# Optimization experiments

Measured on AMD Instinct MI355X. Metric: run time of the kernel, lower is better.

Reference implementation:

```python
import jax, jax.numpy as jnp
import numpy as np
from jax import lax

BS, T, H, V, E, NREG, SEQ = 1024, 10, 256, 50000, 50, 1, 50
EPS = 1e-5


def _edge_index(bs):
    # get_batch_graph(max_len=10, windows=3): per graph, edges[0:-1] of combinations keeps
    # (j-3, j-2) and (j-3, j-1) for j in 3..10, plus (8,9) and (9,0). 18 edges/graph.
    e = []
    for j in range(3, 11):
        e += [(j - 3, j - 2), (j - 3, j - 1)]
    e += [(8, 9), (9, 0)]
    e = np.asarray(e, dtype=np.int32)                      # [18, 2]
    e = (e[None] + 10 * np.arange(bs, dtype=np.int32)[:, None, None]).reshape(-1, 2)
    return jnp.asarray(e[:, 0]), jnp.asarray(e[:, 1])      # src, dst


def setup_inputs() -> dict:
    key = jax.random.key(0)
    ks = jax.random.split(key, 24)
    s = 0.02
    inp = {
        'lags': jax.random.normal(ks[0], (BS, T), jnp.float32),
        'weather': jax.random.normal(ks[1], (BS, T, 2), jnp.float32),
        'event': jax.random.normal(ks[2], (BS, T, 4), jnp.float32),
        'text': jax.random.randint(ks[3], (BS, T, SEQ), 0, V, jnp.int32),
        'emb': jax.random.normal(ks[4], (V, E), jnp.float32) * s,
        'conv3_w': jax.random.normal(ks[5], (H // 2, E, 3), jnp.float32) * s,
        'conv3_b': jnp.zeros((H // 2,), jnp.float32),
        'conv4_w': jax.random.normal(ks[6], (H // 2, H // 2, 4), jnp.float32) * s,
        'conv4_b': jnp.zeros((H // 2,), jnp.float32),
        'lags_w': jax.random.normal(ks[7], (H, 1), jnp.float32) * s,
        'lags_b': jnp.zeros((H,), jnp.float32),
        'weather_w': jax.random.normal(ks[8], (H, 2), jnp.float32) * s,
        'weather_b': jnp.zeros((H,), jnp.float32),
        'event_w': jax.random.normal(ks[9], (H, 4), jnp.float32) * s,
        'event_b': jnp.zeros((H,), jnp.float32),
        'text_w': jax.random.normal(ks[10], (H, H // 2), jnp.float32) * s,
        'text_b': jnp.zeros((H,), jnp.float32),
        'merge_w': jax.random.normal(ks[11], (H, 4 * H), jnp.float32) * s,
        'merge_b': jnp.zeros((H,), jnp.float32),
        'bn_gamma': jnp.ones((H,), jnp.float32),
        'bn_beta': jnp.zeros((H,), jnp.float32),
        'mh_w': jax.random.normal(ks[12], (H, H), jnp.float32) * s,
        'mh_b': jnp.zeros((H,), jnp.float32),
        'gru_wih': jax.random.normal(ks[13], (3 * H, H), jnp.float32) * s,
        'gru_whh': jax.random.normal(ks[14], (3 * H, H), jnp.float32) * s,
        'gru_bih': jnp.zeros((3 * H,), jnp.float32),
        'gru_bhh': jnp.zeros((3 * H,), jnp.float32),
        'reg_w': jax.random.normal(ks[15], (NREG, T * H), jnp.float32) * s,
        'reg_b': jnp.zeros((NREG,), jnp.float32),
    }
    return inp


def _conv1d(x, w, b):
    # x: [N, Cin, L], w: [Cout, Cin, K] (torch layout)
    y = lax.conv_general_dilated(x, w, (1,), 'VALID',
                                 dimension_numbers=('NCH', 'OIH', 'NCH'))
    return y + b[None, :, None]


def _forward(lags, weather, event, text, emb, conv3_w, conv3_b, conv4_w, conv4_b,
             lags_w, lags_b, weather_w, weather_b, event_w, event_b, text_w, text_b,
             merge_w, merge_b, bn_gamma, bn_beta, mh_w, mh_b,
             gru_wih, gru_whh, gru_bih, gru_bhh, reg_w, reg_b):
    bs = lags.shape[0]
    n = bs * T
    h = mh_w.shape[0]

    # per-node feature projections
    l = lags.reshape(-1, 1) @ lags_w.T + lags_b                       # [N, H]
    w = weather.reshape(-1, 2) @ weather_w.T + weather_b              # [N, H]
    ev = event.reshape(-1, 4) @ event_w.T + event_b                   # [N, H]

    # text CNN branch (dropout = identity, eval mode)
    tx = emb[text.reshape(-1, SEQ)]                                   # [N, 50, E]
    tx = jnp.transpose(tx, (0, 2, 1))                                 # [N, E, 50]
    c3 = jax.nn.relu(_conv1d(tx, conv3_w, conv3_b))                   # [N, H/2, 48]
    c4 = jax.nn.relu(_conv1d(c3, conv4_w, conv4_b))                   # [N, H/2, 45]
    tx = jnp.max(c4, axis=2)                                          # [N, H/2]
    tx = tx @ text_w.T + text_b                                       # [N, H]

    # message passing: sum mailbox per destination node (all nodes have in-deg >= 1)
    src, dst = _edge_index(bs)
    def agg(f):
        return jax.ops.segment_sum(f[src], dst, num_segments=n)
    hcat = jnp.concatenate([agg(l), agg(w), agg(ev), agg(tx)], axis=-1)  # [N, 4H]

    # fused linear -> relu -> batchnorm (batch stats) -> linear
    m = jax.nn.relu(hcat @ merge_w.T + merge_b)
    mu = jnp.mean(m, axis=0)
    var = jnp.var(m, axis=0)
    m = (m - mu) / jnp.sqrt(var + EPS) * bn_gamma + bn_beta
    m = m @ mh_w.T + mh_b                                             # [N, H]

    # GRU over the 10 lag steps
    hg = m.reshape(bs, T, h)
    def step(hprev, x_t):
        gi = x_t @ gru_wih.T + gru_bih
        gh = hprev @ gru_whh.T + gru_bhh
        r = jax.nn.sigmoid(gi[:, :h] + gh[:, :h])
        z = jax.nn.sigmoid(gi[:, h:2 * h] + gh[:, h:2 * h])
        nn_ = jnp.tanh(gi[:, 2 * h:] + r * gh[:, 2 * h:])
        hnew = (1.0 - z) * nn_ + z * hprev
        return hnew, hnew
    h0 = jnp.zeros((bs, h), m.dtype)
    _, outs = lax.scan(step, h0, jnp.transpose(hg, (1, 0, 2)))        # [T, bs, H]
    out = jnp.transpose(outs, (1, 0, 2)).reshape(bs, -1)              # [bs, T*H]
    return out @ reg_w.T + reg_b                                      # [bs, n_reg]


def reference(lags, weather, event, text, emb, conv3_w, conv3_b, conv4_w, conv4_b,
              lags_w, lags_b, weather_w, weather_b, event_w, event_b, text_w, text_b,
              merge_w, merge_b, bn_gamma, bn_beta, mh_w, mh_b,
              gru_wih, gru_whh, gru_bih, gru_bhh, reg_w, reg_b):
    return _forward(lags, weather, event, text, emb, conv3_w, conv3_b, conv4_w, conv4_b,
                    lags_w, lags_b, weather_w, weather_b, event_w, event_b, text_w, text_b,
                    merge_w, merge_b, bn_gamma, bn_beta, mh_w, mh_b,
                    gru_wih, gru_whh, gru_bih, gru_bhh, reg_w, reg_b)
```

## Files before the change

### kernel.cpp

```cpp
#include <hip/hip_runtime.h>
#include <math.h>


typedef unsigned short u16;
typedef __attribute__((ext_vector_type(8))) short short8v;
typedef __attribute__((ext_vector_type(4))) float float4v;
#define MFMA16 __builtin_amdgcn_mfma_f32_16x16x32_bf16

__device__ inline u16 f2bf(float f) {
  unsigned u = __float_as_uint(f);
  u += 0x7FFFu + ((u >> 16) & 1u);
  return (u16)(u >> 16);
}

__global__ __launch_bounds__(256) void k_zero(float* __restrict__ p, int n) {
  int i = blockIdx.x * 256 + threadIdx.x;
  if (i < n) p[i] = 0.f;
}

__global__ __launch_bounds__(256) void k_repb3(const float* __restrict__ w3,
                                               u16* __restrict__ w3b) {
  int i = blockIdx.x * 256 + threadIdx.x;
  if (i >= 24576) return;
  int j = i & 7, l = (i >> 3) & 63, nt = (i >> 9) & 7, kt = i >> 12;
  int k = kt * 32 + (l >> 4) * 8 + j;
  int c = nt * 16 + (l & 15);
  int kk = k >> 6, e = k & 63;
  float v = (e < 50) ? w3[c * 150 + e * 3 + kk] : 0.f;
  w3b[i] = f2bf(v);
}

__global__ __launch_bounds__(256) void k_repb4(const float* __restrict__ w4,
                                               u16* __restrict__ w4b) {
  int i = blockIdx.x * 256 + threadIdx.x;
  int j = i & 7, l = (i >> 3) & 63, nt = (i >> 9) & 7, kt = i >> 12;
  int k = kt * 32 + (l >> 4) * 8 + j;
  int c = nt * 16 + (l & 15);
  int kk = k >> 7, ci = k & 127;
  w4b[i] = f2bf(w4[c * 512 + ci * 4 + kk]);
}

__global__ __launch_bounds__(256) void k_repwhh(const float* __restrict__ whh,
                                                u16* __restrict__ whhb) {
  int i = blockIdx.x * 256 + threadIdx.x;
  int j = i & 7, l = (i >> 3) & 63, kt = (i >> 9) & 7, nt = i >> 12;
  int n = nt * 16 + (l & 15);
  int k = kt * 32 + (l >> 4) * 8 + j;
  whhb[i] = f2bf(whh[n * 256 + k]);
}

__global__ __launch_bounds__(256) void k_pcomb(const float* __restrict__ wih,
                                               const float* __restrict__ mh_w,
                                               const float* __restrict__ mh_b,
                                               const float* __restrict__ bih,
                                               float* __restrict__ Wcomb,
                                               float* __restrict__ b1) {
  int g0 = blockIdx.x * 8, t = threadIdx.x;
  float acc[8] = {0.f, 0.f, 0.f, 0.f, 0.f, 0.f, 0.f, 0.f};
  for (int j = 0; j < 256; ++j) {
    float wv = mh_w[j * 256 + t];
#pragma unroll
    for (int r = 0; r < 8; ++r) acc[r] += wih[(g0 + r) * 256 + j] * wv;
  }
#pragma unroll
  for (int r = 0; r < 8; ++r) Wcomb[(g0 + r) * 256 + t] = acc[r];
  __shared__ float red[4][8];
  float mb = mh_b[t];
#pragma unroll
  for (int r = 0; r < 8; ++r) {
    float v = wih[(g0 + r) * 256 + t] * mb;
    v += __shfl_down(v, 32); v += __shfl_down(v, 16); v += __shfl_down(v, 8);
    v += __shfl_down(v, 4);  v += __shfl_down(v, 2);  v += __shfl_down(v, 1);
    if ((t & 63) == 0) red[t >> 6][r] = v;
  }
  __syncthreads();
  if (t < 8) b1[g0 + t] = bih[g0 + t] + red[0][t] + red[1][t] + red[2][t] + red[3][t];
}

__global__ __launch_bounds__(256) void k_pmerge(const float* __restrict__ merge_w,
                                                const float* __restrict__ text_w,
                                                const float* __restrict__ lags_w,
                                                const float* __restrict__ weather_w,
                                                const float* __restrict__ event_w,
                                                const float* __restrict__ lags_b,
                                                const float* __restrict__ weather_b,
                                                const float* __restrict__ event_b,
                                                const float* __restrict__ text_b,
                                                float* __restrict__ MtxT,
                                                float* __restrict__ A_l,
                                                float* __restrict__ MwT,
                                                float* __restrict__ MeT,
                                                float* __restrict__ bias_deg) {
  int blk = blockIdx.x, t = threadIdx.x;
  if (blk < 128) {
    int c = blk;
    float acc = 0.f;
    for (int j = 0; j < 256; ++j)
      acc += merge_w[t * 1024 + 768 + j] * text_w[j * 128 + c];
    MtxT[c * 256 + t] = acc;
  } else {
    float a = 0.f, w0 = 0.f, w1 = 0.f, e0 = 0.f, e1 = 0.f, e2 = 0.f, e3 = 0.f, bd = 0.f;
    for (int j = 0; j < 256; ++j) {
      float m0 = merge_w[t * 1024 + j];
      float m1 = merge_w[t * 1024 + 256 + j];
      float m2 = merge_w[t * 1024 + 512 + j];
      float m3 = merge_w[t * 1024 + 768 + j];
      a  += m0 * lags_w[j];
      w0 += m1 * weather_w[j * 2 + 0];
      w1 += m1 * weather_w[j * 2 + 1];
      e0 += m2 * event_w[j * 4 + 0];
      e1 += m2 * event_w[j * 4 + 1];
      e2 += m2 * event_w[j * 4 + 2];
      e3 += m2 * event_w[j * 4 + 3];
      bd += m0 * lags_b[j] + m1 * weather_b[j] + m2 * event_b[j] + m3 * text_b[j];
    }
    A_l[t] = a;
    MwT[t] = w0; MwT[256 + t] = w1;
    MeT[t] = e0; MeT[256 + t] = e1; MeT[512 + t] = e2; MeT[768 + t] = e3;
    bias_deg[t] = bd;
  }
}


#define LOADB(DST, SRC, KT)                                                    \
  _Pragma("unroll") for (int nt = 0; nt < 8; ++nt)                             \
      DST[nt] = *(const short8v*)&SRC[((((KT) * 8 + nt) * 64) + l) * 8];

#define AFRAG3(AF, KT) {                                                       \
    const int kk_ = (KT) >> 1;                                                 \
    const int eb_ = 4 * ((KT) & 1) + g;                                        \
    _Pragma("unroll") for (int mt = 0; mt < 3; ++mt) {                         \
      int pr_ = 16 * mt + lr + kk_;                                            \
      int bb_ = eb_ ^ (pr_ & 7);                                               \
      AF[mt] = *(const short8v*)&sx[pr_ * 64 + bb_ * 8];                       \
    } }

#define AFRAG4(AF, KT) {                                                       \
    const int t4_ = 4 * (KT) + g;                                              \
    const int kk_ = t4_ >> 4;                                                  \
    const int bk_ = t4_ & 15;                                                  \
    _Pragma("unroll") for (int mt = 0; mt < 3; ++mt) {                         \
      int pr_ = 16 * mt + lr + kk_;                                            \
      int bb_ = (bk_ & 8) | ((bk_ ^ pr_) & 7);                                 \
      AF[mt] = *(const short8v*)&sc3[pr_ * 128 + bb_ * 8];                     \
    } }

#define MSTEP(AF, BF)                                                          \
  _Pragma("unroll") for (int nt = 0; nt < 8; ++nt)                             \
    _Pragma("unroll") for (int mt = 0; mt < 3; ++mt)                           \
      acc[mt][nt] = MFMA16(AF[mt], BF[nt], acc[mt][nt], 0, 0, 0);

__global__ __launch_bounds__(64) void k_textcnn(const int* __restrict__ text,
                                                const float* __restrict__ emb,
                                                const u16* __restrict__ w3b,
                                                const float* __restrict__ b3,
                                                const u16* __restrict__ w4b,
                                                const float* __restrict__ b4,
                                                float* __restrict__ mx_g) {
  __shared__ u16 sbuf[52 * 128];
  u16* sx = sbuf;
  u16* sc3 = sbuf;
  const int n = blockIdx.x;
  const int l = threadIdx.x;
  const int lr = l & 15;
  const int g = l >> 4;

  int idxv = (l < 50) ? text[n * 50 + l] : 0;
  const int e = l;
#pragma unroll 10
  for (int s = 0; s < 50; ++s) {
    int id = __shfl(idxv, s);
    float v = (e < 50) ? emb[id * 50 + e] : 0.f;
    int bb = (e >> 3) ^ (s & 7);
    sx[s * 64 + bb * 8 + (e & 7)] = f2bf(v);
  }
  __syncthreads();

  const float4v zv = {0.f, 0.f, 0.f, 0.f};
  float4v acc[3][8];
#pragma unroll
  for (int mt = 0; mt < 3; ++mt)
#pragma unroll
    for (int nt = 0; nt < 8; ++nt) acc[mt][nt] = zv;

  float b3v[8];
#pragma unroll
  for (int nt = 0; nt < 8; ++nt) b3v[nt] = b3[nt * 16 + lr];

  {
    short8v bA[8], bB[8], a[3];
    LOADB(bA, w3b, 0);
    for (int kt = 0; kt < 6; kt += 2) {
      LOADB(bB, w3b, kt + 1);
      AFRAG3(a, kt);
      MSTEP(a, bA);
      if (kt + 2 < 6) LOADB(bA, w3b, kt + 2);
      AFRAG3(a, kt + 1);
      MSTEP(a, bB);
    }
  }
  __syncthreads();

#pragma unroll
  for (int mt = 0; mt < 3; ++mt)
#pragma unroll
    for (int nt = 0; nt < 8; ++nt) {
#pragma unroll
      for (int r = 0; r < 4; ++r) {
        int p = 16 * mt + 4 * g + r;
        int c = 16 * nt + lr;
        float v = fmaxf(acc[mt][nt][r] + b3v[nt], 0.f);
        int bb = (c >> 3) & 15;
        bb = (bb & 8) | ((bb ^ (p & 7)) & 7);
        sc3[p * 128 + bb * 8 + (c & 7)] = f2bf(v);
      }
      acc[mt][nt] = zv;
    }
  __syncthreads();

  {
    short8v bA[8], bB[8], a[3];
    LOADB(bA, w4b, 0);
    for (int kt = 0; kt < 16; kt += 2) {
      LOADB(bB, w4b, kt + 1);
      AFRAG4(a, kt);
      MSTEP(a, bA);
      if (kt + 2 < 16) LOADB(bA, w4b, kt + 2);
      AFRAG4(a, kt + 1);
      MSTEP(a, bB);
    }
  }

#pragma unroll
  for (int nt = 0; nt < 8; ++nt) {
    float m0 = -1e30f;
#pragma unroll
    for (int mt = 0; mt < 3; ++mt)
#pragma unroll
      for (int r = 0; r < 4; ++r) {
        int p = 16 * mt + 4 * g + r;
        if (p < 45) m0 = fmaxf(m0, acc[mt][nt][r]);
      }
    m0 = fmaxf(m0, __shfl_xor(m0, 16));
    m0 = fmaxf(m0, __shfl_xor(m0, 32));
    int c = 16 * nt + lr;
    float bias = b4[c];
    if (g == 0) mx_g[n * 128 + c] = fmaxf(m0 + bias, 0.f);
  }
}

__device__ inline void preds_of(int i, int& p1, int& p2, int& d) {
  int tt = i % 10;
  int base = i - tt;
  if (tt == 0)      { p1 = base + 9;      p2 = -1;             d = 1; }
  else if (tt == 1) { p1 = base;          p2 = -1;             d = 1; }
  else              { p1 = base + tt - 2; p2 = base + tt - 1;  d = 2; }
}

__global__ __launch_bounds__(256) void k_merge(const float* __restrict__ mx_g,
                                               const float* __restrict__ lags,
                                               const float* __restrict__ weather,
                                               const float* __restrict__ event,
                                               const float* __restrict__ MtxT,
                                               const float* __restrict__ A_l,
                                               const float* __restrict__ MwT,
                                               const float* __restrict__ MeT,
                                               const float* __restrict__ bias_deg,
                                               const float* __restrict__ merge_b,
                                               u16* __restrict__ m_bf,
                                               float* __restrict__ bnsum,
                                               float* __restrict__ bnsumsq) {
  __shared__ __align__(16) float mxs[16 * 128];
  __shared__ float scal[16 * 8];
  const int tid = threadIdx.x;
  const int row0 = blockIdx.x * 16;
  for (int idx = tid; idx < 2048; idx += 256) {
    int r = idx >> 7, c = idx & 127;
    int p1, p2, d;
    preds_of(row0 + r, p1, p2, d);
    float v = mx_g[p1 * 128 + c];
    if (p2 >= 0) v += mx_g[p2 * 128 + c];
    mxs[r * 128 + c] = v;
  }
  if (tid < 16) {
    int p1, p2, d;
    preds_of(row0 + tid, p1, p2, d);
    float sl = lags[p1];
    float sw0 = weather[p1 * 2], sw1 = weather[p1 * 2 + 1];
    float se0 = event[p1 * 4], se1 = event[p1 * 4 + 1];
    float se2 = event[p1 * 4 + 2], se3 = event[p1 * 4 + 3];
    if (p2 >= 0) {
      sl += lags[p2];
      sw0 += weather[p2 * 2]; sw1 += weather[p2 * 2 + 1];
      se0 += event[p2 * 4];     se1 += event[p2 * 4 + 1];
      se2 += event[p2 * 4 + 2]; se3 += event[p2 * 4 + 3];
    }
    scal[tid * 8 + 0] = sl;
    scal[tid * 8 + 1] = sw0; scal[tid * 8 + 2] = sw1;
    scal[tid * 8 + 3] = se0; scal[tid * 8 + 4] = se1;
    scal[tid * 8 + 5] = se2; scal[tid * 8 + 6] = se3;
    scal[tid * 8 + 7] = (float)d;
  }
  __syncthreads();
  const int t = tid;
  float acc[16];
#pragma unroll
  for (int r = 0; r < 16; ++r) acc[r] = 0.f;
  for (int c4 = 0; c4 < 32; ++c4) {
    const int c = c4 * 4;
    float w0 = MtxT[c * 256 + t];
    float w1 = MtxT[(c + 1) * 256 + t];
    float w2 = MtxT[(c + 2) * 256 + t];
    float w3 = MtxT[(c + 3) * 256 + t];
#pragma unroll
    for (int r = 0; r < 16; ++r) {
      float4 mv = *(const float4*)&mxs[r * 128 + c];
      acc[r] += mv.x * w0 + mv.y * w1 + mv.z * w2 + mv.w * w3;
    }
  }
  float al = A_l[t], mw0 = MwT[t], mw1 = MwT[256 + t];
  float me0 = MeT[t], me1 = MeT[256 + t], me2 = MeT[512 + t], me3 = MeT[768 + t];
  float bd = bias_deg[t], mb = merge_b[t];
  float s1 = 0.f, s2 = 0.f;
#pragma unroll
  for (int r = 0; r < 16; ++r) {
    float mp = acc[r] + scal[r * 8] * al + scal[r * 8 + 1] * mw0 + scal[r * 8 + 2] * mw1
             + scal[r * 8 + 3] * me0 + scal[r * 8 + 4] * me1 + scal[r * 8 + 5] * me2
             + scal[r * 8 + 6] * me3 + scal[r * 8 + 7] * bd + mb;
    float mv = fmaxf(mp, 0.f);
    m_bf[(row0 + r) * 256 + t] = f2bf(mv);
    s1 += mv;
    s2 += mv * mv;
  }
  atomicAdd(&bnsum[t], s1);
  atomicAdd(&bnsumsq[t], s2);
}

__global__ __launch_bounds__(256) void k_bna(const float* __restrict__ bnsum,
                                             const float* __restrict__ bnsumsq,
                                             const float* __restrict__ gamma,
                                             const float* __restrict__ beta,
                                             float* __restrict__ svec,
                                             float* __restrict__ tvec) {
  int c = threadIdx.x;
  float mu = bnsum[c] * (1.f / 10240.f);
  float var = bnsumsq[c] * (1.f / 10240.f) - mu * mu;
  float s = gamma[c] * rsqrtf(var + 1e-5f);
  svec[c] = s;
  tvec[c] = beta[c] - mu * s;
}

__global__ __launch_bounds__(256) void k_bnbc(const float* __restrict__ Wcomb,
                                              const float* __restrict__ svec,
                                              const float* __restrict__ tvec,
                                              const float* __restrict__ b1,
                                              u16* __restrict__ wbig_b,
                                              float* __restrict__ bias_big) {
  int blk = blockIdx.x, t = threadIdx.x;
  __shared__ float red[4];
  if (blk < 768) {
    int i = blk * 256 + t;
    int j = i & 7, l = (i >> 3) & 63, kt = (i >> 9) & 7, nt = i >> 12;
    int n = nt * 16 + (l & 15);
    int k = kt * 32 + (l >> 4) * 8 + j;
    wbig_b[i] = f2bf(Wcomb[n * 256 + k] * svec[k]);
  } else {
    int gg = blk - 768;
    float part = tvec[t] * Wcomb[gg * 256 + t];
    part += __shfl_down(part, 32); part += __shfl_down(part, 16);
    part += __shfl_down(part, 8);  part += __shfl_down(part, 4);
    part += __shfl_down(part, 2);  part += __shfl_down(part, 1);
    if ((t & 63) == 0) red[t >> 6] = part;
    __syncthreads();
    if (t == 0) bias_big[gg] = b1[gg] + red[0] + red[1] + red[2] + red[3];
  }
}

__global__ __launch_bounds__(256) void k_gi(const u16* __restrict__ m_bf,
                                            const u16* __restrict__ wbig_b,
                                            const float* __restrict__ bias_big,
                                            float* __restrict__ gi) {
  const int t = threadIdx.x;
  const int w = t >> 6, l = t & 63, lr = l & 15, g = l >> 4;
  const int row0 = blockIdx.x * 16;
  short8v a[8];
#pragma unroll
  for (int kt = 0; kt < 8; ++kt)
    a[kt] = *(const short8v*)&m_bf[(row0 + lr) * 256 + kt * 32 + g * 8];
  const float4v zv = {0.f, 0.f, 0.f, 0.f};
  float4v acc[12];
#pragma unroll
  for (int j = 0; j < 12; ++j) acc[j] = zv;
#pragma unroll 2
  for (int kt = 0; kt < 8; ++kt) {
#pragma unroll
    for (int j = 0; j < 12; ++j) {
      int nt = w * 12 + j;
      short8v b = *(const short8v*)&wbig_b[((nt * 8 + kt) * 64 + l) * 8];
      acc[j] = MFMA16(a[kt], b, acc[j], 0, 0, 0);
    }
  }
#pragma unroll
  for (int j = 0; j < 12; ++j) {
    int col = (w * 12 + j) * 16 + lr;
    float bb = bias_big[col];
#pragma unroll
    for (int r = 0; r < 4; ++r)
      gi[(row0 + g * 4 + r) * 768 + col] = acc[j][r] + bb;
  }
}

__global__ __launch_bounds__(256) void k_gru_all(const float* __restrict__ gi,
                                                 const u16* __restrict__ whhb,
                                                 const float* __restrict__ bhh,
                                                 const float* __restrict__ reg_w,
                                                 const float* __restrict__ reg_b,
                                                 float* __restrict__ out) {
  __shared__ u16 hb[16 * 256];
  __shared__ float red[4][16];
  const int t = threadIdx.x;
  const int w = t >> 6, l = t & 63, lr = l & 15, g = l >> 4;
  const int row0 = blockIdx.x * 16;
  for (int i = t; i < 4096; i += 256) hb[i] = 0;
  float hp[4][4];
#pragma unroll
  for (int i = 0; i < 4; ++i)
#pragma unroll
    for (int r = 0; r < 4; ++r) hp[i][r] = 0.f;
  float bh[3][4];
#pragma unroll
  for (int gate = 0; gate < 3; ++gate)
#pragma unroll
    for (int i = 0; i < 4; ++i)
      bh[gate][i] = bhh[gate * 256 + (w * 4 + i) * 16 + lr];
  float racc[4] = {0.f, 0.f, 0.f, 0.f};

  for (int s = 0; s < 10; ++s) {
    __syncthreads();
    const float4v zv = {0.f, 0.f, 0.f, 0.f};
    float4v acc[3][4];
#pragma unroll
    for (int gate = 0; gate < 3; ++gate)
#pragma unroll
      for (int i = 0; i < 4; ++i) acc[gate][i] = zv;
#pragma unroll
    for (int kt = 0; kt < 8; ++kt) {
      int kb = kt * 4 + g;
      int bb = kb ^ (lr & 7);
      short8v a = *(const short8v*)&hb[lr * 256 + bb * 8];
#pragma unroll
      for (int gate = 0; gate < 3; ++gate)
#pragma unroll
        for (int i = 0; i < 4; ++i) {
          int nt = gate * 16 + w * 4 + i;
          short8v b = *(const short8v*)&whhb[((nt * 8 + kt) * 64 + l) * 8];
          acc[gate][i] = MFMA16(a, b, acc[gate][i], 0, 0, 0);
        }
    }
    __syncthreads();
    float rw[4];
#pragma unroll
    for (int i = 0; i < 4; ++i) rw[i] = reg_w[s * 256 + (w * 4 + i) * 16 + lr];
#pragma unroll
    for (int i = 0; i < 4; ++i) {
      int c = (w * 4 + i) * 16 + lr;
#pragma unroll
      for (int r = 0; r < 4; ++r) {
        int node = (row0 + g * 4 + r) * 10 + s;
        float gir = gi[node * 768 + c];
        float giz = gi[node * 768 + 256 + c];
        float gin = gi[node * 768 + 512 + c];
        float ghr = acc[0][i][r] + bh[0][i];
        float ghz = acc[1][i][r] + bh[1][i];
        float ghn = acc[2][i][r] + bh[2][i];
        float rg = 1.f / (1.f + expf(-(gir + ghr)));
        float zg = 1.f / (1.f + expf(-(giz + ghz)));
        float ng = tanhf(gin + rg * ghn);
        float hn = (1.f - zg) * ng + zg * hp[i][r];
        hp[i][r] = hn;
        racc[r] += hn * rw[i];
        int m = g * 4 + r;
        int bb2 = (c >> 3) ^ (m & 7);
        hb[m * 256 + bb2 * 8 + (c & 7)] = f2bf(hn);
      }
    }
  }
#pragma unroll
  for (int r = 0; r < 4; ++r) {
    float v = racc[r];
    v += __shfl_xor(v, 1); v += __shfl_xor(v, 2);
    v += __shfl_xor(v, 4); v += __shfl_xor(v, 8);
    racc[r] = v;
  }
  if (lr == 0) {
#pragma unroll
    for (int r = 0; r < 4; ++r) red[w][g * 4 + r] = racc[r];
  }
  __syncthreads();
  if (t < 16)
    out[row0 + t] = reg_b[0] + red[0][t] + red[1][t] + red[2][t] + red[3][t];
}

extern "C" void kernel_launch(void* const* d_in, const int* in_sizes, int n_in,
                              void* d_out, int out_size, void* d_ws, size_t ws_size,
                              hipStream_t stream) {
  (void)in_sizes; (void)n_in; (void)out_size; (void)ws_size;
  const float* lags      = (const float*)d_in[0];
  const float* weather   = (const float*)d_in[1];
  const float* event     = (const float*)d_in[2];
  const int*   text      = (const int*)d_in[3];
  const float* emb       = (const float*)d_in[4];
  const float* conv3_w   = (const float*)d_in[5];
  const float* conv3_b   = (const float*)d_in[6];
  const float* conv4_w   = (const float*)d_in[7];
  const float* conv4_b   = (const float*)d_in[8];
  const float* lags_w    = (const float*)d_in[9];
  const float* lags_b    = (const float*)d_in[10];
  const float* weather_w = (const float*)d_in[11];
  const float* weather_b = (const float*)d_in[12];
  const float* event_w   = (const float*)d_in[13];
  const float* event_b   = (const float*)d_in[14];
  const float* text_w    = (const float*)d_in[15];
  const float* text_b    = (const float*)d_in[16];
  const float* merge_w   = (const float*)d_in[17];
  const float* merge_b   = (const float*)d_in[18];
  const float* bn_gamma  = (const float*)d_in[19];
  const float* bn_beta   = (const float*)d_in[20];
  const float* mh_w      = (const float*)d_in[21];
  const float* mh_b      = (const float*)d_in[22];
  const float* gru_wih   = (const float*)d_in[23];
  const float* gru_whh   = (const float*)d_in[24];
  const float* gru_bih   = (const float*)d_in[25];
  const float* gru_bhh   = (const float*)d_in[26];
  const float* reg_w     = (const float*)d_in[27];
  const float* reg_b     = (const float*)d_in[28];
  float* out = (float*)d_out;

  float* p = (float*)d_ws;
  float* bnsum    = p; p += 256;
  float* bnsumsq  = p; p += 256;
  float* mx       = p; p += 10240 * 128;
  u16*   m_bf     = (u16*)p; p += 10240 * 128;
  float* gi       = p; p += 10240 * 768;
  u16*   w3b      = (u16*)p; p += 12288;
  u16*   w4b      = (u16*)p; p += 32768;
  u16*   whhb     = (u16*)p; p += 98304;
  u16*   wbig_b   = (u16*)p; p += 98304;
  float* Wcomb    = p; p += 196608;
  float* MtxT     = p; p += 32768;
  float* A_l      = p; p += 256;
  float* MwT      = p; p += 512;
  float* MeT      = p; p += 1024;
  float* bias_deg = p; p += 256;
  float* b1       = p; p += 768;
  float* bias_big = p; p += 768;
  float* svec     = p; p += 256;
  float* tvec     = p; p += 256;

  k_zero<<<dim3(2), dim3(256), 0, stream>>>(bnsum, 512);
  k_repb3<<<dim3(96), dim3(256), 0, stream>>>(conv3_w, w3b);
  k_repb4<<<dim3(256), dim3(256), 0, stream>>>(conv4_w, w4b);
  k_repwhh<<<dim3(768), dim3(256), 0, stream>>>(gru_whh, whhb);
  k_pcomb<<<dim3(96), dim3(256), 0, stream>>>(gru_wih, mh_w, mh_b, gru_bih, Wcomb, b1);
  k_pmerge<<<dim3(129), dim3(256), 0, stream>>>(merge_w, text_w, lags_w, weather_w, event_w,
                                                lags_b, weather_b, event_b, text_b,
                                                MtxT, A_l, MwT, MeT, bias_deg);
  k_textcnn<<<dim3(10240), dim3(64), 0, stream>>>(text, emb, w3b, conv3_b, w4b, conv4_b, mx);
  k_merge<<<dim3(640), dim3(256), 0, stream>>>(mx, lags, weather, event, MtxT, A_l, MwT, MeT,
                                               bias_deg, merge_b, m_bf, bnsum, bnsumsq);
  k_bna<<<dim3(1), dim3(256), 0, stream>>>(bnsum, bnsumsq, bn_gamma, bn_beta, svec, tvec);
  k_bnbc<<<dim3(1536), dim3(256), 0, stream>>>(Wcomb, svec, tvec, b1, wbig_b, bias_big);
  k_gi<<<dim3(640), dim3(256), 0, stream>>>(m_bf, wbig_b, bias_big, gi);
  k_gru_all<<<dim3(64), dim3(256), 0, stream>>>(gi, whhb, gru_bhh, reg_w, reg_b, out);
}
```

Before: 668.7 us.

## Split textcnn output channels across two wavefronts per block

The text CNN kernel now uses 128 threads (two wavefronts) per sentence instead of one, and each wave computes half of the 128 output channels for both conv layers. The embedding gather is also split, with each wave loading 25 of the 50 tokens. This halves the per-wave accumulator and B-fragment registers, which can raise occupancy and latency hiding. In exchange, the A fragments are read from shared memory by both waves, and per-block sync overhead goes up.

```diff
diff --git a/kernel.cpp b/kernel.cpp
--- a/kernel.cpp
+++ b/kernel.cpp
@@ -122,9 +122,9 @@
 }
 
 
-#define LOADB(DST, SRC, KT)                                                    \
-  _Pragma("unroll") for (int nt = 0; nt < 8; ++nt)                             \
-      DST[nt] = *(const short8v*)&SRC[((((KT) * 8 + nt) * 64) + l) * 8];
+#define LOADB4(DST, SRC, KT)                                                   \
+  _Pragma("unroll") for (int q = 0; q < 4; ++q)                                \
+      DST[q] = *(const short8v*)&SRC[((((KT) * 8 + NB + q) * 64) + l) * 8];
 
 #define AFRAG3(AF, KT) {                                                       \
     const int kk_ = (KT) >> 1;                                                 \
@@ -145,31 +145,35 @@
       AF[mt] = *(const short8v*)&sc3[pr_ * 128 + bb_ * 8];                     \
     } }
 
-#define MSTEP(AF, BF)                                                          \
-  _Pragma("unroll") for (int nt = 0; nt < 8; ++nt)                             \
+#define MSTEP4(AF, BF)                                                         \
+  _Pragma("unroll") for (int q = 0; q < 4; ++q)                                \
     _Pragma("unroll") for (int mt = 0; mt < 3; ++mt)                           \
-      acc[mt][nt] = MFMA16(AF[mt], BF[nt], acc[mt][nt], 0, 0, 0);
-
-__global__ __launch_bounds__(64) void k_textcnn(const int* __restrict__ text,
-                                                const float* __restrict__ emb,
-                                                const u16* __restrict__ w3b,
-                                                const float* __restrict__ b3,
-                                                const u16* __restrict__ w4b,
-                                                const float* __restrict__ b4,
-                                                float* __restrict__ mx_g) {
+      acc[mt][q] = MFMA16(AF[mt], BF[q], acc[mt][q], 0, 0, 0);
+
+__global__ __launch_bounds__(128) void k_textcnn(const int* __restrict__ text,
+                                                 const float* __restrict__ emb,
+                                                 const u16* __restrict__ w3b,
+                                                 const float* __restrict__ b3,
+                                                 const u16* __restrict__ w4b,
+                                                 const float* __restrict__ b4,
+                                                 float* __restrict__ mx_g) {
   __shared__ u16 sbuf[52 * 128];
   u16* sx = sbuf;
   u16* sc3 = sbuf;
   const int n = blockIdx.x;
-  const int l = threadIdx.x;
+  const int t = threadIdx.x;
+  const int wv = t >> 6;
+  const int l = t & 63;
   const int lr = l & 15;
   const int g = l >> 4;
-
-  int idxv = (l < 50) ? text[n * 50 + l] : 0;
+  const int NB = wv * 4;
+
+  int idxv = (l < 25) ? text[n * 50 + wv * 25 + l] : 0;
   const int e = l;
-#pragma unroll 10
-  for (int s = 0; s < 50; ++s) {
-    int id = __shfl(idxv, s);
+#pragma unroll 5
+  for (int si = 0; si < 25; ++si) {
+    int s = wv * 25 + si;
+    int id = __shfl(idxv, si);
     float v = (e < 50) ? emb[id * 50 + e] : 0.f;
     int bb = (e >> 3) ^ (s & 7);
     sx[s * 64 + bb * 8 + (e & 7)] = f2bf(v);
@@ -177,26 +181,26 @@
   __syncthreads();
 
   const float4v zv = {0.f, 0.f, 0.f, 0.f};
-  float4v acc[3][8];
+  float4v acc[3][4];
 #pragma unroll
   for (int mt = 0; mt < 3; ++mt)
 #pragma unroll
-    for (int nt = 0; nt < 8; ++nt) acc[mt][nt] = zv;
-
-  float b3v[8];
-#pragma unroll
-  for (int nt = 0; nt < 8; ++nt) b3v[nt] = b3[nt * 16 + lr];
+    for (int q = 0; q < 4; ++q) acc[mt][q] = zv;
+
+  float b3v[4];
+#pragma unroll
+  for (int q = 0; q < 4; ++q) b3v[q] = b3[(NB + q) * 16 + lr];
 
   {
-    short8v bA[8], bB[8], a[3];
-    LOADB(bA, w3b, 0);
+    short8v bA[4], bB[4], a[3];
+    LOADB4(bA, w3b, 0);
     for (int kt = 0; kt < 6; kt += 2) {
-      LOADB(bB, w3b, kt + 1);
+      LOADB4(bB, w3b, kt + 1);
       AFRAG3(a, kt);
-      MSTEP(a, bA);
-      if (kt + 2 < 6) LOADB(bA, w3b, kt + 2);
+      MSTEP4(a, bA);
+      if (kt + 2 < 6) LOADB4(bA, w3b, kt + 2);
       AFRAG3(a, kt + 1);
-      MSTEP(a, bB);
+      MSTEP4(a, bB);
     }
   }
   __syncthreads();
@@ -204,46 +208,46 @@
 #pragma unroll
   for (int mt = 0; mt < 3; ++mt)
 #pragma unroll
-    for (int nt = 0; nt < 8; ++nt) {
+    for (int q = 0; q < 4; ++q) {
 #pragma unroll
       for (int r = 0; r < 4; ++r) {
         int p = 16 * mt + 4 * g + r;
-        int c = 16 * nt + lr;
-        float v = fmaxf(acc[mt][nt][r] + b3v[nt], 0.f);
+        int c = (NB + q) * 16 + lr;
+        float v = fmaxf(acc[mt][q][r] + b3v[q], 0.f);
         int bb = (c >> 3) & 15;
         bb = (bb & 8) | ((bb ^ (p & 7)) & 7);
         sc3[p * 128 + bb * 8 + (c & 7)] = f2bf(v);
       }
-      acc[mt][nt] = zv;
+      acc[mt][q] = zv;
     }
   __syncthreads();
 
   {
-    short8v bA[8], bB[8], a[3];
-    LOADB(bA, w4b, 0);
+    short8v bA[4], bB[4], a[3];
+    LOADB4(bA, w4b, 0);
     for (int kt = 0; kt < 16; kt += 2) {
-      LOADB(bB, w4b, kt + 1);
+      LOADB4(bB, w4b, kt + 1);
       AFRAG4(a, kt);
-      MSTEP(a, bA);
-      if (kt + 2 < 16) LOADB(bA, w4b, kt + 2);
+      MSTEP4(a, bA);
+      if (kt + 2 < 16) LOADB4(bA, w4b, kt + 2);
       AFRAG4(a, kt + 1);
-      MSTEP(a, bB);
-    }
-  }
-
-#pragma unroll
-  for (int nt = 0; nt < 8; ++nt) {
+      MSTEP4(a, bB);
+    }
+  }
+
+#pragma unroll
+  for (int q = 0; q < 4; ++q) {
     float m0 = -1e30f;
 #pragma unroll
     for (int mt = 0; mt < 3; ++mt)
 #pragma unroll
       for (int r = 0; r < 4; ++r) {
         int p = 16 * mt + 4 * g + r;
-        if (p < 45) m0 = fmaxf(m0, acc[mt][nt][r]);
+        if (p < 45) m0 = fmaxf(m0, acc[mt][q][r]);
       }
     m0 = fmaxf(m0, __shfl_xor(m0, 16));
     m0 = fmaxf(m0, __shfl_xor(m0, 32));
-    int c = 16 * nt + lr;
+    int c = (NB + q) * 16 + lr;
     float bias = b4[c];
     if (g == 0) mx_g[n * 128 + c] = fmaxf(m0 + bias, 0.f);
   }
@@ -565,7 +569,7 @@
   k_pmerge<<<dim3(129), dim3(256), 0, stream>>>(merge_w, text_w, lags_w, weather_w, event_w,
                                                 lags_b, weather_b, event_b, text_b,
                                                 MtxT, A_l, MwT, MeT, bias_deg);
-  k_textcnn<<<dim3(10240), dim3(64), 0, stream>>>(text, emb, w3b, conv3_b, w4b, conv4_b, mx);
+  k_textcnn<<<dim3(10240), dim3(128), 0, stream>>>(text, emb, w3b, conv3_b, w4b, conv4_b, mx);
   k_merge<<<dim3(640), dim3(256), 0, stream>>>(mx, lags, weather, event, MtxT, A_l, MwT, MeT,
                                                bias_deg, merge_b, m_bf, bnsum, bnsumsq);
   k_bna<<<dim3(1), dim3(256), 0, stream>>>(bnsum, bnsumsq, bn_gamma, bn_beta, svec, tvec);
```

Result: faster. 618.8 us (-7.5%).
